# Optimization experiments

Measured on AMD Instinct MI355X. Metric: run time of the kernel, lower is better.

The kernel has to match this reference:

```python
import jax, jax.numpy as jnp
import numpy as np

B, T, C, H = 2, 2048, 1024, 16  # batch, seq, d_model, heads
D = C // H                       # head dim = 64


def setup_inputs() -> dict:
    key = jax.random.key(0)
    ks = jax.random.split(key, 5)
    s = 0.02  # init scale for weights
    return {
        "x": jax.random.normal(ks[0], (B, T, C), jnp.float32),
        "Wq": jax.random.normal(ks[1], (C, C), jnp.float32) * s,
        "bq": jnp.zeros((C,), jnp.float32),
        "Wk": jax.random.normal(ks[2], (C, C), jnp.float32) * s,
        "bk": jnp.zeros((C,), jnp.float32),
        "Wv": jax.random.normal(ks[3], (C, C), jnp.float32) * s,
        "bv": jnp.zeros((C,), jnp.float32),
        "Wo": jax.random.normal(ks[4], (C, C), jnp.float32) * s,
        "bo": jnp.zeros((C,), jnp.float32),
    }


def reference(x, Wq, bq, Wk, bk, Wv, bv, Wo, bo):
    b, t, c = x.shape
    h, d = H, C // H
    # QKV projections (torch Linear: x @ W.T + b), split into heads: b h t d
    q = (x @ Wq.T + bq).reshape(b, t, h, d).transpose(0, 2, 1, 3)
    k = (x @ Wk.T + bk).reshape(b, t, h, d).transpose(0, 2, 1, 3)
    v = (x @ Wv.T + bv).reshape(b, t, h, d).transpose(0, 2, 1, 3)

    scale = 1.0 / float(np.sqrt(d))
    att = jnp.einsum("bhqd,bhkd->bhqk", q, k) * scale  # [B,H,T,T]
    causal = jnp.tril(jnp.ones((t, t), dtype=bool))
    att = jnp.where(causal[None, None, :, :], att, -jnp.inf)
    att = jax.nn.softmax(att, axis=-1)
    att_weights = att  # attn_dropout with p=0 is identity

    y = jnp.einsum("bhqk,bhkd->bhqd", att, v)          # [B,H,T,D]
    y = y.transpose(0, 2, 1, 3).reshape(b, t, c)        # b q (h d)
    y = y @ Wo.T + bo                                   # out proj; resid_dropout p=0
    return y, att_weights
```

## Files before the change

kernel.cpp:

```cpp
#include <hip/hip_runtime.h>

#define DI __device__ __forceinline__

typedef __attribute__((ext_vector_type(8))) short short8;
typedef __attribute__((ext_vector_type(4))) float floatx4;
typedef unsigned short u16;

#define Bb 2
#define Tt 2048
#define Cc 1024
#define Hh 16
#define Dd 64
#define C1 0.1803368801111244f
#define NEGBIG (-1e30f)

DI float bf2f(u16 u) { union { unsigned int i; float f; } v; v.i = ((unsigned int)u) << 16; return v.f; }
DI u16 f2bf(float f) {
  union { float f; unsigned int i; } v; v.f = f;
  unsigned int i = v.i;
  unsigned int r = i + 0x7fffu + ((i >> 16) & 1u);
  return (u16)(r >> 16);
}

DI floatx4 mfma16(short8 a, short8 b, floatx4 c) {
  return __builtin_amdgcn_mfma_f32_16x16x32_bf16(a, b, c, 0, 0, 0);
}

DI void gload16(const u16* g, u16* l) {
  __builtin_amdgcn_global_load_lds(
      (const __attribute__((address_space(1))) unsigned int*)(g),
      (__attribute__((address_space(3))) unsigned int*)(l), 16, 0, 0);
}

DI uint4 load8(const void* p, size_t eoff, int isbf) {
  if (isbf) {
    return *(const uint4*)((const u16*)p + eoff);
  } else {
    const float* f = (const float*)p + eoff;
    float4 a = *(const float4*)f;
    float4 b = *(const float4*)(f + 4);
    union { uint4 u; u16 s[8]; } r;
    r.s[0] = f2bf(a.x); r.s[1] = f2bf(a.y); r.s[2] = f2bf(a.z); r.s[3] = f2bf(a.w);
    r.s[4] = f2bf(b.x); r.s[5] = f2bf(b.y); r.s[6] = f2bf(b.z); r.s[7] = f2bf(b.w);
    return r.u;
  }
}

DI float loadb(const void* p, int i, int isbf) {
  return isbf ? bf2f(((const u16*)p)[i]) : ((const float*)p)[i];
}

__global__ void detect_dtype(const u16* __restrict__ x, int* __restrict__ flag) {
  __shared__ int cnt[256];
  int c = 0;
  for (int i = threadIdx.x; i < 4096; i += 256) {
    unsigned u = x[2 * i];
    unsigned e = (u >> 7) & 0xFFu;
    c += (e == 0u || (e >= 100u && e <= 150u)) ? 1 : 0;
  }
  cnt[threadIdx.x] = c;
  __syncthreads();
  for (int s = 128; s > 0; s >>= 1) {
    if ((int)threadIdx.x < s) cnt[threadIdx.x] += cnt[threadIdx.x + s];
    __syncthreads();
  }
  if (threadIdx.x == 0) *flag = (cnt[0] > 2458) ? 1 : 0;
}

__global__ __launch_bounds__(256) void convert_all(
    const void* __restrict__ x,
    const void* __restrict__ wq, const void* __restrict__ wk,
    const void* __restrict__ wv, const void* __restrict__ wo,
    u16* __restrict__ xb,
    u16* __restrict__ wqb, u16* __restrict__ wkb,
    u16* __restrict__ wvb, u16* __restrict__ wob,
    const int* __restrict__ flagp) {
  const int isbf = *flagp;
  const void* src;
  u16* dst;
  size_t n;
  switch (blockIdx.y) {
    case 0: src = x;  dst = xb;  n = (size_t)Bb * Tt * Cc; break;
    case 1: src = wq; dst = wqb; n = (size_t)Cc * Cc; break;
    case 2: src = wk; dst = wkb; n = (size_t)Cc * Cc; break;
    case 3: src = wv; dst = wvb; n = (size_t)Cc * Cc; break;
    default: src = wo; dst = wob; n = (size_t)Cc * Cc; break;
  }
  size_t i8 = ((size_t)blockIdx.x * 256 + threadIdx.x) * 8;
  size_t step = (size_t)gridDim.x * 256 * 8;
  for (; i8 < n; i8 += step) {
    uint4 v = load8(src, i8, isbf);
    *(uint4*)(dst + i8) = v;
  }
}

__global__ __launch_bounds__(256) void qkv_gemm(
    const u16* __restrict__ Xb,
    const u16* __restrict__ Wqb, const u16* __restrict__ Wkb, const u16* __restrict__ Wvb,
    const void* __restrict__ bq, const void* __restrict__ bk, const void* __restrict__ bv,
    u16* __restrict__ Qb, u16* __restrict__ Kb, u16* __restrict__ Vb,
    const int* __restrict__ flagp) {
  __shared__ __align__(16) u16 As[128 * 32];
  __shared__ __align__(16) u16 Bs[128 * 32];
  const int isbf = *flagp;
  const int z = blockIdx.z;
  const u16* W = (z == 0) ? Wqb : (z == 1) ? Wkb : Wvb;
  const void* bias = (z == 0) ? bq : (z == 1) ? bk : bv;
  u16* Out = (z == 0) ? Qb : (z == 1) ? Kb : Vb;

  const int m0 = blockIdx.y * 128, n0 = blockIdx.x * 128;
  const int tid = threadIdx.x;
  const int w = tid >> 6, lane = tid & 63, quad = lane >> 4, l15 = lane & 15;
  const int wm = w >> 1, wn = w & 1;

  floatx4 acc[4][4];
#pragma unroll
  for (int a = 0; a < 4; ++a)
#pragma unroll
    for (int b2 = 0; b2 < 4; ++b2) acc[a][b2] = (floatx4){0.f, 0.f, 0.f, 0.f};

  const int s0 = w * 128 + lane, s1 = s0 + 64;
  const int rA0 = s0 >> 2, c0 = (s0 & 3) * 8;
  const int rA1 = s1 >> 2, c1 = (s1 & 3) * 8;
  const u16* gA0 = Xb + (size_t)(m0 + rA0) * Cc + c0;
  const u16* gA1 = Xb + (size_t)(m0 + rA1) * Cc + c1;
  const u16* gB0 = W + (size_t)(n0 + rA0) * Cc + c0;
  const u16* gB1 = W + (size_t)(n0 + rA1) * Cc + c1;
  u16* lA0 = As + w * 1024;
  u16* lA1 = As + w * 1024 + 512;
  u16* lB0 = Bs + w * 1024;
  u16* lB1 = Bs + w * 1024 + 512;

  for (int k0 = 0; k0 < Cc; k0 += 32) {
    __syncthreads();
    gload16(gA0 + k0, lA0);
    gload16(gA1 + k0, lA1);
    gload16(gB0 + k0, lB0);
    gload16(gB1 + k0, lB1);
    __syncthreads();
    short8 af[4], bfv[4];
#pragma unroll
    for (int t = 0; t < 4; ++t)
      af[t] = *(const short8*)(As + (wm * 64 + t * 16 + l15) * 32 + quad * 8);
#pragma unroll
    for (int t = 0; t < 4; ++t)
      bfv[t] = *(const short8*)(Bs + (wn * 64 + t * 16 + l15) * 32 + quad * 8);
#pragma unroll
    for (int tm = 0; tm < 4; ++tm)
#pragma unroll
      for (int tn = 0; tn < 4; ++tn) acc[tm][tn] = mfma16(af[tm], bfv[tn], acc[tm][tn]);
  }

  float bb[4];
#pragma unroll
  for (int tn = 0; tn < 4; ++tn) bb[tn] = loadb(bias, n0 + wn * 64 + tn * 16 + l15, isbf);
#pragma unroll
  for (int tm = 0; tm < 4; ++tm) {
#pragma unroll
    for (int tn = 0; tn < 4; ++tn) {
      int n = n0 + wn * 64 + tn * 16 + l15;
      int h = n >> 6, d = n & 63;
#pragma unroll
      for (int r = 0; r < 4; ++r) {
        int m = m0 + wm * 64 + tm * 16 + quad * 4 + r;
        int b = m >> 11, t = m & 2047;
        Out[(((size_t)(b * Hh + h) * Tt) + t) * Dd + d] = f2bf(acc[tm][tn][r] + bb[tn]);
      }
    }
  }
}

__global__ __launch_bounds__(256) void out_gemm(
    const u16* __restrict__ Y, const u16* __restrict__ Wob, const void* __restrict__ bo,
    float* __restrict__ Out, const int* __restrict__ flagp) {
  __shared__ __align__(16) u16 As[128 * 32];
  __shared__ __align__(16) u16 Bs[128 * 32];
  const int isbf = *flagp;
  const int m0 = blockIdx.y * 128, n0 = blockIdx.x * 128;
  const int tid = threadIdx.x;
  const int w = tid >> 6, lane = tid & 63, quad = lane >> 4, l15 = lane & 15;
  const int wm = w >> 1, wn = w & 1;

  floatx4 acc[4][4];
#pragma unroll
  for (int a = 0; a < 4; ++a)
#pragma unroll
    for (int b2 = 0; b2 < 4; ++b2) acc[a][b2] = (floatx4){0.f, 0.f, 0.f, 0.f};

  const int s0 = w * 128 + lane, s1 = s0 + 64;
  const int rA0 = s0 >> 2, c0 = (s0 & 3) * 8;
  const int rA1 = s1 >> 2, c1 = (s1 & 3) * 8;
  const u16* gA0 = Y + (size_t)(m0 + rA0) * Cc + c0;
  const u16* gA1 = Y + (size_t)(m0 + rA1) * Cc + c1;
  const u16* gB0 = Wob + (size_t)(n0 + rA0) * Cc + c0;
  const u16* gB1 = Wob + (size_t)(n0 + rA1) * Cc + c1;
  u16* lA0 = As + w * 1024;
  u16* lA1 = As + w * 1024 + 512;
  u16* lB0 = Bs + w * 1024;
  u16* lB1 = Bs + w * 1024 + 512;

  for (int k0 = 0; k0 < Cc; k0 += 32) {
    __syncthreads();
    gload16(gA0 + k0, lA0);
    gload16(gA1 + k0, lA1);
    gload16(gB0 + k0, lB0);
    gload16(gB1 + k0, lB1);
    __syncthreads();
    short8 af[4], bfv[4];
#pragma unroll
    for (int t = 0; t < 4; ++t)
      af[t] = *(const short8*)(As + (wm * 64 + t * 16 + l15) * 32 + quad * 8);
#pragma unroll
    for (int t = 0; t < 4; ++t)
      bfv[t] = *(const short8*)(Bs + (wn * 64 + t * 16 + l15) * 32 + quad * 8);
#pragma unroll
    for (int tm = 0; tm < 4; ++tm)
#pragma unroll
      for (int tn = 0; tn < 4; ++tn) acc[tm][tn] = mfma16(af[tm], bfv[tn], acc[tm][tn]);
  }

  float bb[4];
#pragma unroll
  for (int tn = 0; tn < 4; ++tn) bb[tn] = loadb(bo, n0 + wn * 64 + tn * 16 + l15, isbf);
#pragma unroll
  for (int tm = 0; tm < 4; ++tm)
#pragma unroll
    for (int tn = 0; tn < 4; ++tn) {
      int n = n0 + wn * 64 + tn * 16 + l15;
#pragma unroll
      for (int r = 0; r < 4; ++r) {
        int m = m0 + wm * 64 + tm * 16 + quad * 4 + r;
        Out[(size_t)m * Cc + n] = acc[tm][tn][r] + bb[tn];
      }
    }
}

__global__ __launch_bounds__(512) void attn_kernel(
    const u16* __restrict__ Qbuf, const u16* __restrict__ Kbuf, const u16* __restrict__ Vbuf,
    float* __restrict__ Att, u16* __restrict__ Ybuf) {
  __shared__ __align__(16) u16 Vts[2][64 * 136];
  __shared__ __align__(16) u16 Ps[8 * 16 * 40];

  const int id = blockIdx.x;
  const int zp = id >> 5;
  const int hb = id & 31;
  const int b = hb >> 4, h = hb & 15;

  const int tid = threadIdx.x;
  const int w = tid >> 6, lane = tid & 63, quad = lane >> 4, l15 = lane & 15;

  const size_t headoff = (size_t)(b * Hh + h) * Tt * Dd;
  const u16* Qh = Qbuf + headoff;
  const u16* Kh = Kbuf + headoff;
  const u16* Vh = Vbuf + headoff;
  float* attO = Att + (size_t)(b * Hh + h) * Tt * Tt;
  u16* Psw = Ps + w * 640;

  const u16* Kl = Kh + (size_t)l15 * Dd + quad * 8;
  const int vrow = tid >> 2, vcb = (tid & 3) * 16;

  for (int half = 0; half < 2; ++half) {
    const int qt = half ? (15 - zp) : zp;
    const int q0 = qt * 128;
    const int qw = q0 + w * 16;

    short8 aq0 = *(const short8*)(Qh + (size_t)(qw + l15) * Dd + quad * 8);
    short8 aq1 = *(const short8*)(Qh + (size_t)(qw + l15) * Dd + 32 + quad * 8);

    float m4[4], l4[4];
#pragma unroll
    for (int r = 0; r < 4; ++r) { m4[r] = NEGBIG; l4[r] = 0.f; }

    for (int c = 0; c <= qt; ++c) {
      const int kb = c * 128;
      floatx4 s[8];
#pragma unroll
      for (int kt = 0; kt < 8; ++kt) {
        const u16* kp = Kl + (size_t)(kb + kt * 16) * Dd;
        short8 b0 = *(const short8*)(kp);
        short8 b1 = *(const short8*)(kp + 32);
        floatx4 t = (floatx4){0.f, 0.f, 0.f, 0.f};
        t = mfma16(aq0, b0, t);
        t = mfma16(aq1, b1, t);
        s[kt] = t;
      }
      const bool partial = (kb + 127 > qw);
#pragma unroll
      for (int r = 0; r < 4; ++r) {
        const int qi = qw + quad * 4 + r;
        float e[8];
        float bm = NEGBIG;
#pragma unroll
        for (int kt = 0; kt < 8; ++kt) {
          float s2 = s[kt][r] * C1;
          if (partial) {
            int key = kb + kt * 16 + l15;
            s2 = (key <= qi) ? s2 : NEGBIG;
          }
          e[kt] = s2;
          bm = fmaxf(bm, s2);
        }
        float mn = fmaxf(m4[r], bm);
        float sum = 0.f;
#pragma unroll
        for (int kt = 0; kt < 8; ++kt) sum += exp2f(e[kt] - mn);
        l4[r] = l4[r] * exp2f(m4[r] - mn) + sum;
        m4[r] = mn;
      }
    }
#pragma unroll
    for (int r = 0; r < 4; ++r) {
      float m = m4[r], l = l4[r];
#pragma unroll
      for (int off = 1; off <= 8; off <<= 1) {
        float mo = __shfl_xor(m, off, 64);
        float lo = __shfl_xor(l, off, 64);
        float mn = fmaxf(m, mo);
        l = l * exp2f(m - mn) + lo * exp2f(mo - mn);
        m = mn;
      }
      m4[r] = m; l4[r] = l;
    }
    float lrec[4];
#pragma unroll
    for (int r = 0; r < 4; ++r) lrec[r] = 1.0f / l4[r];

    floatx4 yacc[4];
#pragma unroll
    for (int dt = 0; dt < 4; ++dt) yacc[dt] = (floatx4){0.f, 0.f, 0.f, 0.f};

    uint4 va = *(const uint4*)(Vh + (size_t)vrow * Dd + vcb);
    uint4 vb = *(const uint4*)(Vh + (size_t)vrow * Dd + vcb + 8);

    for (int c = 0; c <= qt; ++c) {
      const int kb = c * 128;
      u16* Vt = &Vts[c & 1][0];
      {
        union { uint4 u; u16 sv[8]; } cv;
        cv.u = va;
#pragma unroll
        for (int j = 0; j < 8; ++j) Vt[(vcb + j) * 136 + vrow] = cv.sv[j];
        cv.u = vb;
#pragma unroll
        for (int j = 0; j < 8; ++j) Vt[(vcb + 8 + j) * 136 + vrow] = cv.sv[j];
      }
      if (c < qt) {
        va = *(const uint4*)(Vh + (size_t)(kb + 128 + vrow) * Dd + vcb);
        vb = *(const uint4*)(Vh + (size_t)(kb + 128 + vrow) * Dd + vcb + 8);
      }

      floatx4 s[8];
#pragma unroll
      for (int kt = 0; kt < 8; ++kt) {
        const u16* kp = Kl + (size_t)(kb + kt * 16) * Dd;
        short8 b0 = *(const short8*)(kp);
        short8 b1 = *(const short8*)(kp + 32);
        floatx4 t = (floatx4){0.f, 0.f, 0.f, 0.f};
        t = mfma16(aq0, b0, t);
        t = mfma16(aq1, b1, t);
        s[kt] = t;
      }

      __syncthreads();

      const bool partial = (kb + 127 > qw);
#pragma unroll
      for (int ks = 0; ks < 4; ++ks) {
#pragma unroll
        for (int kk = 0; kk < 2; ++kk) {
          const int kt = ks * 2 + kk;
#pragma unroll
          for (int r = 0; r < 4; ++r) {
            const int row = quad * 4 + r;
            const int qi = qw + row;
            const int key = kb + kt * 16 + l15;
            float p = exp2f(fminf(s[kt][r] * C1 - m4[r], 0.f)) * lrec[r];
            if (partial && key > qi) p = 0.f;
            attO[(size_t)qi * Tt + key] = p;
            Psw[row * 40 + kk * 16 + l15] = f2bf(p);
          }
        }
        short8 ap = *(const short8*)(Psw + l15 * 40 + quad * 8);
#pragma unroll
        for (int dt = 0; dt < 4; ++dt) {
          short8 bv = *(const short8*)(Vt + (dt * 16 + l15) * 136 + ks * 32 + quad * 8);
          yacc[dt] = mfma16(ap, bv, yacc[dt]);
        }
      }
    }

    {
      uint4 z; z.x = 0u; z.y = 0u; z.z = 0u; z.w = 0u;
      for (int c = qt + 1; c < 16; ++c) {
        const int kb = c * 128;
#pragma unroll
        for (int i = 0; i < 8; ++i) {
          int slot = tid + i * 512;
          int row = slot >> 5, g = slot & 31;
          *(uint4*)(attO + (size_t)(q0 + row) * Tt + kb + g * 4) = z;
        }
      }
    }

#pragma unroll
    for (int dt = 0; dt < 4; ++dt) {
#pragma unroll
      for (int r = 0; r < 4; ++r) {
        const int qi = qw + quad * 4 + r;
        Ybuf[(size_t)(b * Tt + qi) * Cc + h * Dd + dt * 16 + l15] = f2bf(yacc[dt][r]);
      }
    }
  }
}

extern "C" void kernel_launch(void* const* d_in, const int* in_sizes, int n_in,
                              void* d_out, int out_size, void* d_ws, size_t ws_size,
                              hipStream_t stream) {
  const void* x  = d_in[0];
  const void* Wq = d_in[1];
  const void* bq = d_in[2];
  const void* Wk = d_in[3];
  const void* bk = d_in[4];
  const void* Wv = d_in[5];
  const void* bv = d_in[6];
  const void* Wo = d_in[7];
  const void* bo = d_in[8];
  float* out = (float*)d_out;

  const size_t NTC = (size_t)Bb * Tt * Cc;
  const size_t CC = (size_t)Cc * Cc;

  char* wsb = (char*)d_ws;
  int* flag = (int*)wsb;
  u16* Qb = (u16*)(wsb + 256);
  u16* Kb = Qb + NTC;
  u16* Vb = Kb + NTC;
  u16* Yb = Vb + NTC;
  u16* Xb = Yb + NTC;
  u16* Wqb = Xb + NTC;
  u16* Wkb = Wqb + CC;
  u16* Wvb = Wkb + CC;
  u16* Wob = Wvb + CC;

  hipLaunchKernelGGL(detect_dtype, dim3(1), dim3(256), 0, stream, (const u16*)x, flag);
  hipLaunchKernelGGL(convert_all, dim3(512, 5), dim3(256), 0, stream,
                     x, Wq, Wk, Wv, Wo, Xb, Wqb, Wkb, Wvb, Wob, flag);
  hipLaunchKernelGGL(qkv_gemm, dim3(8, 32, 3), dim3(256), 0, stream,
                     Xb, Wqb, Wkb, Wvb, bq, bk, bv, Qb, Kb, Vb, flag);
  float* attOut = out + NTC;
  hipLaunchKernelGGL(attn_kernel, dim3(256), dim3(512), 0, stream,
                     Qb, Kb, Vb, attOut, Yb);
  hipLaunchKernelGGL(out_gemm, dim3(8, 32, 1), dim3(256), 0, stream,
                     Yb, Wob, bo, out, flag);
}
```

Baseline: 751.7 us.

## Launch one block per query tile and stage K tiles through shared memory

```diff
diff --git a/kernel.cpp b/kernel.cpp
--- a/kernel.cpp
+++ b/kernel.cpp
@@ -238,11 +238,12 @@
 __global__ __launch_bounds__(512) void attn_kernel(
     const u16* __restrict__ Qbuf, const u16* __restrict__ Kbuf, const u16* __restrict__ Vbuf,
     float* __restrict__ Att, u16* __restrict__ Ybuf) {
-  __shared__ __align__(16) u16 Vts[2][64 * 136];
+  __shared__ __align__(16) u16 Ks[128 * 72];
+  __shared__ __align__(16) u16 Vts[64 * 136];
   __shared__ __align__(16) u16 Ps[8 * 16 * 40];
 
   const int id = blockIdx.x;
-  const int zp = id >> 5;
+  const int qt = 15 - (id >> 5);
   const int hb = id & 31;
   const int b = hb >> 4, h = hb & 15;
 
@@ -256,159 +257,167 @@
   float* attO = Att + (size_t)(b * Hh + h) * Tt * Tt;
   u16* Psw = Ps + w * 640;
 
-  const u16* Kl = Kh + (size_t)l15 * Dd + quad * 8;
+  const int q0 = qt * 128;
+  const int qw = q0 + w * 16;
+
   const int vrow = tid >> 2, vcb = (tid & 3) * 16;
 
-  for (int half = 0; half < 2; ++half) {
-    const int qt = half ? (15 - zp) : zp;
-    const int q0 = qt * 128;
-    const int qw = q0 + w * 16;
-
-    short8 aq0 = *(const short8*)(Qh + (size_t)(qw + l15) * Dd + quad * 8);
-    short8 aq1 = *(const short8*)(Qh + (size_t)(qw + l15) * Dd + 32 + quad * 8);
-
-    float m4[4], l4[4];
-#pragma unroll
-    for (int r = 0; r < 4; ++r) { m4[r] = NEGBIG; l4[r] = 0.f; }
-
-    for (int c = 0; c <= qt; ++c) {
+  short8 aq0 = *(const short8*)(Qh + (size_t)(qw + l15) * Dd + quad * 8);
+  short8 aq1 = *(const short8*)(Qh + (size_t)(qw + l15) * Dd + 32 + quad * 8);
+
+  float m4[4], l4[4];
+#pragma unroll
+  for (int r = 0; r < 4; ++r) { m4[r] = NEGBIG; l4[r] = 0.f; }
+
+  for (int c = 0; c <= qt; ++c) {
+    const int kb = c * 128;
+    __syncthreads();
+#pragma unroll
+    for (int i = 0; i < 2; ++i) {
+      int slot = tid + i * 512;
+      int rr = slot >> 3, g = slot & 7;
+      *(uint4*)(Ks + rr * 72 + g * 8) = *(const uint4*)(Kh + (size_t)(kb + rr) * Dd + g * 8);
+    }
+    __syncthreads();
+
+    floatx4 s[8];
+#pragma unroll
+    for (int kt = 0; kt < 8; ++kt) {
+      short8 b0 = *(const short8*)(Ks + (kt * 16 + l15) * 72 + quad * 8);
+      short8 b1 = *(const short8*)(Ks + (kt * 16 + l15) * 72 + 32 + quad * 8);
+      floatx4 t = (floatx4){0.f, 0.f, 0.f, 0.f};
+      t = mfma16(aq0, b0, t);
+      t = mfma16(aq1, b1, t);
+      s[kt] = t;
+    }
+    const bool partial = (kb + 127 > qw);
+#pragma unroll
+    for (int r = 0; r < 4; ++r) {
+      const int qi = qw + quad * 4 + r;
+      float e[8];
+      float bm = NEGBIG;
+#pragma unroll
+      for (int kt = 0; kt < 8; ++kt) {
+        float s2 = s[kt][r] * C1;
+        if (partial) {
+          int key = kb + kt * 16 + l15;
+          s2 = (key <= qi) ? s2 : NEGBIG;
+        }
+        e[kt] = s2;
+        bm = fmaxf(bm, s2);
+      }
+      float mn = fmaxf(m4[r], bm);
+      float sum = 0.f;
+#pragma unroll
+      for (int kt = 0; kt < 8; ++kt) sum += exp2f(e[kt] - mn);
+      l4[r] = l4[r] * exp2f(m4[r] - mn) + sum;
+      m4[r] = mn;
+    }
+  }
+#pragma unroll
+  for (int r = 0; r < 4; ++r) {
+    float m = m4[r], l = l4[r];
+#pragma unroll
+    for (int off = 1; off <= 8; off <<= 1) {
+      float mo = __shfl_xor(m, off, 64);
+      float lo = __shfl_xor(l, off, 64);
+      float mn = fmaxf(m, mo);
+      l = l * exp2f(m - mn) + lo * exp2f(mo - mn);
+      m = mn;
+    }
+    m4[r] = m; l4[r] = l;
+  }
+  float lrec[4];
+#pragma unroll
+  for (int r = 0; r < 4; ++r) lrec[r] = 1.0f / l4[r];
+
+  floatx4 yacc[4];
+#pragma unroll
+  for (int dt = 0; dt < 4; ++dt) yacc[dt] = (floatx4){0.f, 0.f, 0.f, 0.f};
+
+  uint4 va = *(const uint4*)(Vh + (size_t)vrow * Dd + vcb);
+  uint4 vb = *(const uint4*)(Vh + (size_t)vrow * Dd + vcb + 8);
+
+  for (int c = 0; c <= qt; ++c) {
+    const int kb = c * 128;
+    __syncthreads();
+#pragma unroll
+    for (int i = 0; i < 2; ++i) {
+      int slot = tid + i * 512;
+      int rr = slot >> 3, g = slot & 7;
+      *(uint4*)(Ks + rr * 72 + g * 8) = *(const uint4*)(Kh + (size_t)(kb + rr) * Dd + g * 8);
+    }
+    {
+      union { uint4 u; u16 sv[8]; } cv;
+      cv.u = va;
+#pragma unroll
+      for (int j = 0; j < 8; ++j) Vts[(vcb + j) * 136 + vrow] = cv.sv[j];
+      cv.u = vb;
+#pragma unroll
+      for (int j = 0; j < 8; ++j) Vts[(vcb + 8 + j) * 136 + vrow] = cv.sv[j];
+    }
+    if (c < qt) {
+      va = *(const uint4*)(Vh + (size_t)(kb + 128 + vrow) * Dd + vcb);
+      vb = *(const uint4*)(Vh + (size_t)(kb + 128 + vrow) * Dd + vcb + 8);
+    }
+    __syncthreads();
+
+    floatx4 s[8];
+#pragma unroll
+    for (int kt = 0; kt < 8; ++kt) {
+      short8 b0 = *(const short8*)(Ks + (kt * 16 + l15) * 72 + quad * 8);
+      short8 b1 = *(const short8*)(Ks + (kt * 16 + l15) * 72 + 32 + quad * 8);
+      floatx4 t = (floatx4){0.f, 0.f, 0.f, 0.f};
+      t = mfma16(aq0, b0, t);
+      t = mfma16(aq1, b1, t);
+      s[kt] = t;
+    }
+
+    const bool partial = (kb + 127 > qw);
+#pragma unroll
+    for (int ks = 0; ks < 4; ++ks) {
+#pragma unroll
+      for (int kk = 0; kk < 2; ++kk) {
+        const int kt = ks * 2 + kk;
+#pragma unroll
+        for (int r = 0; r < 4; ++r) {
+          const int row = quad * 4 + r;
+          const int qi = qw + row;
+          const int key = kb + kt * 16 + l15;
+          float p = exp2f(fminf(s[kt][r] * C1 - m4[r], 0.f)) * lrec[r];
+          if (partial && key > qi) p = 0.f;
+          attO[(size_t)qi * Tt + key] = p;
+          Psw[row * 40 + kk * 16 + l15] = f2bf(p);
+        }
+      }
+      short8 ap = *(const short8*)(Psw + l15 * 40 + quad * 8);
+#pragma unroll
+      for (int dt = 0; dt < 4; ++dt) {
+        short8 bv = *(const short8*)(Vts + (dt * 16 + l15) * 136 + ks * 32 + quad * 8);
+        yacc[dt] = mfma16(ap, bv, yacc[dt]);
+      }
+    }
+  }
+
+  {
+    uint4 z; z.x = 0u; z.y = 0u; z.z = 0u; z.w = 0u;
+    for (int c = qt + 1; c < 16; ++c) {
       const int kb = c * 128;
-      floatx4 s[8];
-#pragma unroll
-      for (int kt = 0; kt < 8; ++kt) {
-        const u16* kp = Kl + (size_t)(kb + kt * 16) * Dd;
-        short8 b0 = *(const short8*)(kp);
-        short8 b1 = *(const short8*)(kp + 32);
-        floatx4 t = (floatx4){0.f, 0.f, 0.f, 0.f};
-        t = mfma16(aq0, b0, t);
-        t = mfma16(aq1, b1, t);
-        s[kt] = t;
-      }
-      const bool partial = (kb + 127 > qw);
-#pragma unroll
-      for (int r = 0; r < 4; ++r) {
-        const int qi = qw + quad * 4 + r;
-        float e[8];
-        float bm = NEGBIG;
-#pragma unroll
-        for (int kt = 0; kt < 8; ++kt) {
-          float s2 = s[kt][r] * C1;
-          if (partial) {
-            int key = kb + kt * 16 + l15;
-            s2 = (key <= qi) ? s2 : NEGBIG;
-          }
-          e[kt] = s2;
-          bm = fmaxf(bm, s2);
-        }
-        float mn = fmaxf(m4[r], bm);
-        float sum = 0.f;
-#pragma unroll
-        for (int kt = 0; kt < 8; ++kt) sum += exp2f(e[kt] - mn);
-        l4[r] = l4[r] * exp2f(m4[r] - mn) + sum;
-        m4[r] = mn;
-      }
-    }
+#pragma unroll
+      for (int i = 0; i < 8; ++i) {
+        int slot = tid + i * 512;
+        int row = slot >> 5, g = slot & 31;
+        *(uint4*)(attO + (size_t)(q0 + row) * Tt + kb + g * 4) = z;
+      }
+    }
+  }
+
+#pragma unroll
+  for (int dt = 0; dt < 4; ++dt) {
 #pragma unroll
     for (int r = 0; r < 4; ++r) {
-      float m = m4[r], l = l4[r];
-#pragma unroll
-      for (int off = 1; off <= 8; off <<= 1) {
-        float mo = __shfl_xor(m, off, 64);
-        float lo = __shfl_xor(l, off, 64);
-        float mn = fmaxf(m, mo);
-        l = l * exp2f(m - mn) + lo * exp2f(mo - mn);
-        m = mn;
-      }
-      m4[r] = m; l4[r] = l;
-    }
-    float lrec[4];
-#pragma unroll
-    for (int r = 0; r < 4; ++r) lrec[r] = 1.0f / l4[r];
-
-    floatx4 yacc[4];
-#pragma unroll
-    for (int dt = 0; dt < 4; ++dt) yacc[dt] = (floatx4){0.f, 0.f, 0.f, 0.f};
-
-    uint4 va = *(const uint4*)(Vh + (size_t)vrow * Dd + vcb);
-    uint4 vb = *(const uint4*)(Vh + (size_t)vrow * Dd + vcb + 8);
-
-    for (int c = 0; c <= qt; ++c) {
-      const int kb = c * 128;
-      u16* Vt = &Vts[c & 1][0];
-      {
-        union { uint4 u; u16 sv[8]; } cv;
-        cv.u = va;
-#pragma unroll
-        for (int j = 0; j < 8; ++j) Vt[(vcb + j) * 136 + vrow] = cv.sv[j];
-        cv.u = vb;
-#pragma unroll
-        for (int j = 0; j < 8; ++j) Vt[(vcb + 8 + j) * 136 + vrow] = cv.sv[j];
-      }
-      if (c < qt) {
-        va = *(const uint4*)(Vh + (size_t)(kb + 128 + vrow) * Dd + vcb);
-        vb = *(const uint4*)(Vh + (size_t)(kb + 128 + vrow) * Dd + vcb + 8);
-      }
-
-      floatx4 s[8];
-#pragma unroll
-      for (int kt = 0; kt < 8; ++kt) {
-        const u16* kp = Kl + (size_t)(kb + kt * 16) * Dd;
-        short8 b0 = *(const short8*)(kp);
-        short8 b1 = *(const short8*)(kp + 32);
-        floatx4 t = (floatx4){0.f, 0.f, 0.f, 0.f};
-        t = mfma16(aq0, b0, t);
-        t = mfma16(aq1, b1, t);
-        s[kt] = t;
-      }
-
-      __syncthreads();
-
-      const bool partial = (kb + 127 > qw);
-#pragma unroll
-      for (int ks = 0; ks < 4; ++ks) {
-#pragma unroll
-        for (int kk = 0; kk < 2; ++kk) {
-          const int kt = ks * 2 + kk;
-#pragma unroll
-          for (int r = 0; r < 4; ++r) {
-            const int row = quad * 4 + r;
-            const int qi = qw + row;
-            const int key = kb + kt * 16 + l15;
-            float p = exp2f(fminf(s[kt][r] * C1 - m4[r], 0.f)) * lrec[r];
-            if (partial && key > qi) p = 0.f;
-            attO[(size_t)qi * Tt + key] = p;
-            Psw[row * 40 + kk * 16 + l15] = f2bf(p);
-          }
-        }
-        short8 ap = *(const short8*)(Psw + l15 * 40 + quad * 8);
-#pragma unroll
-        for (int dt = 0; dt < 4; ++dt) {
-          short8 bv = *(const short8*)(Vt + (dt * 16 + l15) * 136 + ks * 32 + quad * 8);
-          yacc[dt] = mfma16(ap, bv, yacc[dt]);
-        }
-      }
-    }
-
-    {
-      uint4 z; z.x = 0u; z.y = 0u; z.z = 0u; z.w = 0u;
-      for (int c = qt + 1; c < 16; ++c) {
-        const int kb = c * 128;
-#pragma unroll
-        for (int i = 0; i < 8; ++i) {
-          int slot = tid + i * 512;
-          int row = slot >> 5, g = slot & 31;
-          *(uint4*)(attO + (size_t)(q0 + row) * Tt + kb + g * 4) = z;
-        }
-      }
-    }
-
-#pragma unroll
-    for (int dt = 0; dt < 4; ++dt) {
-#pragma unroll
-      for (int r = 0; r < 4; ++r) {
-        const int qi = qw + quad * 4 + r;
-        Ybuf[(size_t)(b * Tt + qi) * Cc + h * Dd + dt * 16 + l15] = f2bf(yacc[dt][r]);
-      }
+      const int qi = qw + quad * 4 + r;
+      Ybuf[(size_t)(b * Tt + qi) * Cc + h * Dd + dt * 16 + l15] = f2bf(yacc[dt][r]);
     }
   }
 }
@@ -448,7 +457,7 @@
   hipLaunchKernelGGL(qkv_gemm, dim3(8, 32, 3), dim3(256), 0, stream,
                      Xb, Wqb, Wkb, Wvb, bq, bk, bv, Qb, Kb, Vb, flag);
   float* attOut = out + NTC;
-  hipLaunchKernelGGL(attn_kernel, dim3(256), dim3(512), 0, stream,
+  hipLaunchKernelGGL(attn_kernel, dim3(512), dim3(512), 0, stream,
                      Qb, Kb, Vb, attOut, Yb);
   hipLaunchKernelGGL(out_gemm, dim3(8, 32, 1), dim3(256), 0, stream,
                      Yb, Wob, bo, out, flag);
```

Result: faster. 706.5 us (-6.0%).
